# Performance work log

Hardware: AMD Instinct MI355X
Metric: run time of the kernel (lower is better)

The kernel has to match this reference:

```python
import jax, jax.numpy as jnp
import numpy as np

N_NODES = 100000
N_EDGES = 1600000
NUM_GRAPHS = 4096
EPS = 1e-5


def _glorot(key, shape):
    fan_in, fan_out = shape[0], shape[1]
    lim = float(np.sqrt(6.0 / (fan_in + fan_out)))
    return jax.random.uniform(key, shape, jnp.float32, -lim, lim)


def setup_inputs() -> dict:
    key = jax.random.key(0)
    ks = jax.random.split(key, 32)
    inp = {}
    inp['x'] = jax.random.normal(ks[0], (N_NODES, 32), jnp.float32)
    inp['edge_attr'] = jax.random.uniform(ks[1], (N_EDGES, 8), jnp.float32)
    inp['edge_index'] = jax.random.randint(ks[2], (2, N_EDGES), 0, N_NODES, jnp.int32)
    inp['batch'] = jnp.sort(jax.random.randint(ks[3], (N_NODES,), 0, NUM_GRAPHS, jnp.int32))
    inp['num_graphs'] = NUM_GRAPHS
    # node/edge embeddings
    inp['Wn'] = _glorot(ks[4], (32, 64)); inp['bn_'] = jnp.zeros((64,), jnp.float32)
    inp['We'] = _glorot(ks[5], (8, 16)); inp['be_'] = jnp.zeros((16,), jnp.float32)
    # conv1: 2*64+16=144 -> 128 -> 64
    inp['W1a'] = _glorot(ks[6], (144, 128)); inp['b1a'] = jnp.zeros((128,), jnp.float32)
    inp['W1b'] = _glorot(ks[7], (128, 64)); inp['b1b'] = jnp.zeros((64,), jnp.float32)
    # conv2: 2*64+16=144 -> 64 -> 32
    inp['W2a'] = _glorot(ks[8], (144, 64)); inp['b2a'] = jnp.zeros((64,), jnp.float32)
    inp['W2b'] = _glorot(ks[9], (64, 32)); inp['b2b'] = jnp.zeros((32,), jnp.float32)
    # conv3: 2*32+16=80 -> 32 -> 16
    inp['W3a'] = _glorot(ks[10], (80, 32)); inp['b3a'] = jnp.zeros((32,), jnp.float32)
    inp['W3b'] = _glorot(ks[11], (32, 16)); inp['b3b'] = jnp.zeros((16,), jnp.float32)
    # batchnorm affine params
    inp['g1'] = jnp.ones((64,), jnp.float32); inp['beta1'] = jnp.zeros((64,), jnp.float32)
    inp['g2'] = jnp.ones((32,), jnp.float32); inp['beta2'] = jnp.zeros((32,), jnp.float32)
    inp['g3'] = jnp.ones((16,), jnp.float32); inp['beta3'] = jnp.zeros((16,), jnp.float32)
    # final fc 16 -> 12
    inp['Wfc'] = _glorot(ks[12], (16, 12)); inp['bfc'] = jnp.zeros((12,), jnp.float32)
    return inp


def _conv(x, e_emb, src, dst, Wa, ba, Wb, bb, n_nodes):
    # PyG: x_i = x[target]=x[dst], x_j = x[source]=x[src]; message MLP; mean-aggregate at dst
    m = jnp.concatenate([x[dst], x[src], e_emb], axis=1)      # [E, 2*in+edge]
    m = jax.nn.relu(m @ Wa + ba) @ Wb + bb                    # [E, out]
    s = jax.ops.segment_sum(m, dst, num_segments=n_nodes)
    cnt = jax.ops.segment_sum(jnp.ones((m.shape[0], 1), m.dtype), dst, num_segments=n_nodes)
    return s / jnp.maximum(cnt, 1.0)


def _batchnorm(x, g, b):
    mu = jnp.mean(x, axis=0)
    var = jnp.mean(jnp.square(x - mu), axis=0)
    return (x - mu) * jax.lax.rsqrt(var + EPS) * g + b


def reference(x, edge_attr, edge_index, batch, num_graphs,
              Wn, bn_, We, be_, W1a, b1a, W1b, b1b, W2a, b2a, W2b, b2b,
              W3a, b3a, W3b, b3b, g1, beta1, g2, beta2, g3, beta3, Wfc, bfc):
    n_nodes = x.shape[0]
    src, dst = edge_index[0], edge_index[1]
    e_emb = jax.nn.relu(edge_attr @ We + be_)                 # [E, 16]
    h = jax.nn.relu(x @ Wn + bn_)                             # [N, 64]
    h = _conv(h, e_emb, src, dst, W1a, b1a, W1b, b1b, n_nodes)
    h = jax.nn.relu(_batchnorm(h, g1, beta1))
    h = _conv(h, e_emb, src, dst, W2a, b2a, W2b, b2b, n_nodes)
    h = jax.nn.relu(_batchnorm(h, g2, beta2))
    h = _conv(h, e_emb, src, dst, W3a, b3a, W3b, b3b, n_nodes)
    h = jax.nn.relu(_batchnorm(h, g3, beta3))
    # global mean pool per graph
    s = jax.ops.segment_sum(h, batch, num_segments=num_graphs)
    cnt = jax.ops.segment_sum(jnp.ones((n_nodes, 1), h.dtype), batch, num_segments=num_graphs)
    pooled = s / jnp.maximum(cnt, 1.0)                        # [G, 16]
    return jax.nn.sigmoid(pooled @ Wfc + bfc)                 # [G, 12]
```

## Files before the change

### kernel.cpp

```cpp
#include <hip/hip_runtime.h>
#include <hip/hip_bf16.h>
#include <cstdio>


#define N_NODES 100000
#define N_EDGES 1600000
#define NUM_GRAPHS 4096

typedef unsigned short u16;
typedef unsigned int u32;
typedef _Float16 h2 __attribute__((ext_vector_type(2)));

#if defined(__has_builtin)
#if __has_builtin(__builtin_amdgcn_fdot2)
#define DOT2(a, b, c) __builtin_amdgcn_fdot2((a), (b), (c), false)
#endif
#endif
#ifndef DOT2
#define DOT2(a, b, c) ((c) + (float)(a).x * (float)(b).x + (float)(a).y * (float)(b).y)
#endif

__device__ __forceinline__ float b2f(u16 u) { union { u32 i; float f; } c; c.i = ((u32)u) << 16; return c.f; }
__device__ __forceinline__ float b2f_lo(u32 u) { union { u32 i; float f; } c; c.i = u << 16; return c.f; }
__device__ __forceinline__ float b2f_hi(u32 u) { union { u32 i; float f; } c; c.i = u & 0xffff0000u; return c.f; }
__device__ __forceinline__ u16 f2b(float f) {
    __hip_bfloat16 h = __float2bfloat16(f);
    return *reinterpret_cast<u16*>(&h);
}

template <int CPL>
__device__ __forceinline__ void ld_bf16(const u16* base, float out[CPL]) {
    if constexpr (CPL == 1) {
        out[0] = b2f(*base);
    } else {
        u32 v = *(const u32*)base;
        out[0] = b2f_lo(v); out[1] = b2f_hi(v);
    }
}
template <int CPL>
__device__ __forceinline__ void ld_f32(const float* base, float out[CPL]) {
    if constexpr (CPL == 1) {
        out[0] = *base;
    } else {
        float2 v = *(const float2*)base;
        out[0] = v.x; out[1] = v.y;
    }
}

__global__ __launch_bounds__(256) void hist_k(const int* __restrict__ dst, int* __restrict__ hist) {
    int e = blockIdx.x * 256 + threadIdx.x;
    if (e < N_EDGES) atomicAdd(&hist[dst[e]], 1);
}

__global__ __launch_bounds__(256) void scan_part_k(const int* __restrict__ hist,
        int* __restrict__ excl, int* __restrict__ bsum) {
    __shared__ int sm[256];
    int t = threadIdx.x, b = blockIdx.x;
    int base = b * 1024 + t * 4;
    int v0 = (base + 0 < N_NODES) ? hist[base + 0] : 0;
    int v1 = (base + 1 < N_NODES) ? hist[base + 1] : 0;
    int v2 = (base + 2 < N_NODES) ? hist[base + 2] : 0;
    int v3 = (base + 3 < N_NODES) ? hist[base + 3] : 0;
    int tsum = v0 + v1 + v2 + v3;
    sm[t] = tsum;
    __syncthreads();
    for (int o = 1; o < 256; o <<= 1) {
        int x = (t >= o) ? sm[t - o] : 0;
        __syncthreads();
        sm[t] += x;
        __syncthreads();
    }
    int texcl = sm[t] - tsum;
    if (base + 0 < N_NODES) excl[base + 0] = texcl;
    if (base + 1 < N_NODES) excl[base + 1] = texcl + v0;
    if (base + 2 < N_NODES) excl[base + 2] = texcl + v0 + v1;
    if (base + 3 < N_NODES) excl[base + 3] = texcl + v0 + v1 + v2;
    if (t == 255) bsum[b] = sm[255];
}

__global__ __launch_bounds__(256) void scan_top_k(int* __restrict__ bsum, int* __restrict__ boff,
        int nb, int* __restrict__ row_ptr_last) {
    __shared__ int sm[256];
    int t = threadIdx.x;
    int v = (t < nb) ? bsum[t] : 0;
    sm[t] = v;
    __syncthreads();
    for (int o = 1; o < 256; o <<= 1) {
        int x = (t >= o) ? sm[t - o] : 0;
        __syncthreads();
        sm[t] += x;
        __syncthreads();
    }
    if (t < nb) boff[t] = sm[t] - v;
    if (t == 0) *row_ptr_last = sm[255];
}

__global__ __launch_bounds__(256) void scan_add_k(int* __restrict__ excl, const int* __restrict__ boff,
        int* __restrict__ row_ptr, int* __restrict__ cursor) {
    int i = blockIdx.x * 256 + threadIdx.x;
    if (i >= N_NODES) return;
    int s = excl[i] + boff[i >> 10];
    row_ptr[i] = s;
    cursor[i] = s;
}

__global__ __launch_bounds__(256) void scatter_k(const int* __restrict__ src, const int* __restrict__ dst,
        int* __restrict__ cursor, int* __restrict__ sorted_eid, int* __restrict__ srcs) {
    int e = blockIdx.x * 256 + threadIdx.x;
    if (e < N_EDGES) {
        int p = atomicAdd(&cursor[dst[e]], 1);
        sorted_eid[p] = e;
        srcs[p] = src[e];
    }
}

__global__ __launch_bounds__(256) void edge_emb_k(const float* __restrict__ ea,
        const float* __restrict__ We, const float* __restrict__ be,
        const int* __restrict__ sorted_eid, _Float16* __restrict__ e16s) {
    int idx = blockIdx.x * 256 + threadIdx.x;
    if (idx >= N_EDGES * 16) return;
    int p = idx >> 4, k = idx & 15;
    int e = sorted_eid[p];
    float acc = be[k];
#pragma unroll
    for (int j = 0; j < 8; ++j) acc += ea[(size_t)e * 8 + j] * We[j * 16 + k];
    e16s[idx] = (_Float16)fmaxf(acc, 0.f);
}

__global__ __launch_bounds__(256) void node_emb_k(const float* __restrict__ x,
        const float* __restrict__ Wn, const float* __restrict__ bn_, float* __restrict__ h) {
    int idx = blockIdx.x * 256 + threadIdx.x;
    if (idx >= N_NODES * 64) return;
    int v = idx >> 6, c = idx & 63;
    float acc = bn_[c];
    for (int k = 0; k < 32; ++k) acc += x[(size_t)v * 32 + k] * Wn[(size_t)k * 64 + c];
    h[idx] = fmaxf(acc, 0.f);
}

template <int F, int H>
__global__ __launch_bounds__(256) void proj_k(const float* __restrict__ h,
        const float* __restrict__ Wa, const float* __restrict__ ba,
        float* __restrict__ Pd, u16* __restrict__ Ps) {
    constexpr int C2 = 2 * H;
    constexpr int NPB = 256 / C2;
    constexpr int TILE = 16 * NPB;
    __shared__ float hs[TILE][F];
    const int t = threadIdx.x;
    const int grp = t / C2;
    const int c = t % C2;
    const bool is_src = (c >= H);
    const int cc = is_src ? (c - H) : c;
    float w[F];
    const float* wcol = Wa + (size_t)(is_src ? F : 0) * H + cc;
#pragma unroll
    for (int k = 0; k < F; ++k) w[k] = wcol[(size_t)k * H];
    const float bias = is_src ? 0.f : ba[cc];

    for (int v0 = blockIdx.x * TILE; v0 < N_NODES; v0 += gridDim.x * TILE) {
        __syncthreads();
        for (int i = t; i < TILE * F; i += 256) {
            int vv = v0 + i / F;
            hs[i / F][i % F] = (vv < N_NODES) ? h[(size_t)vv * F + (i % F)] : 0.f;
        }
        __syncthreads();
        const int base = grp * 16;
        const int nmax = (N_NODES - v0 - base >= 16) ? 16
                        : (N_NODES - v0 - base > 0 ? N_NODES - v0 - base : 0);
#pragma unroll 2
        for (int n = 0; n < nmax; ++n) {
            const int v = v0 + base + n;
            const float4* hr4 = (const float4*)hs[base + n];
            float a0 = bias, a1 = 0.f, a2 = 0.f, a3 = 0.f;
#pragma unroll
            for (int k4 = 0; k4 < F / 4; ++k4) {
                float4 hv = hr4[k4];
                a0 += hv.x * w[4 * k4 + 0];
                a1 += hv.y * w[4 * k4 + 1];
                a2 += hv.z * w[4 * k4 + 2];
                a3 += hv.w * w[4 * k4 + 3];
            }
            float acc = (a0 + a1) + (a2 + a3);
            if (is_src) Ps[(size_t)v * H + cc] = f2b(acc);
            else        Pd[(size_t)v * H + cc] = acc;
        }
    }
}

template <int H>
__global__ __launch_bounds__(256) void conv_k(
        const int* __restrict__ row_ptr, const int* __restrict__ srcs,
        const _Float16* __restrict__ e16s,
        float* __restrict__ Pd, const u16* __restrict__ Ps,
        const float* __restrict__ Wae) {
    constexpr int SL = (H >= 64) ? 64 : 32;
    constexpr int NPW = 64 / SL;
    constexpr int CPL = H / SL;
    constexpr int NPB = 4 * NPW;
    const int wave = threadIdx.x >> 6, lane = threadIdx.x & 63;
    const int sub = lane / SL;
    const int sl = lane % SL;
    const int c0 = sl * CPL;
    h2 w2h[8][CPL];
#pragma unroll
    for (int k2 = 0; k2 < 8; ++k2)
#pragma unroll
        for (int j = 0; j < CPL; ++j) {
            h2 t;
            t.x = (_Float16)Wae[(2 * k2) * H + c0 + j];
            t.y = (_Float16)Wae[(2 * k2 + 1) * H + c0 + j];
            w2h[k2][j] = t;
        }

    for (int v = blockIdx.x * NPB + wave * NPW + sub; v < N_NODES; v += gridDim.x * NPB) {
        const int vv = (SL == 64) ? __builtin_amdgcn_readfirstlane(v) : v;
        float pd[CPL], acc[CPL];
        ld_f32<CPL>(&Pd[(size_t)vv * H + c0], pd);
#pragma unroll
        for (int j = 0; j < CPL; ++j) acc[j] = 0.f;
        const int p0 = row_ptr[vv], p1 = row_ptr[vv + 1];
        const int deg = p1 - p0;

        auto edge = [&](uint4 ra, uint4 rb, const float ps[CPL]) {
            union { u32 u; h2 h; } cv;
            h2 ev[8];
            cv.u = ra.x; ev[0] = cv.h; cv.u = ra.y; ev[1] = cv.h;
            cv.u = ra.z; ev[2] = cv.h; cv.u = ra.w; ev[3] = cv.h;
            cv.u = rb.x; ev[4] = cv.h; cv.u = rb.y; ev[5] = cv.h;
            cv.u = rb.z; ev[6] = cv.h; cv.u = rb.w; ev[7] = cv.h;
            float z[CPL];
#pragma unroll
            for (int j = 0; j < CPL; ++j) z[j] = pd[j] + ps[j];
#pragma unroll
            for (int k2 = 0; k2 < 8; ++k2)
#pragma unroll
                for (int j = 0; j < CPL; ++j) z[j] = DOT2(ev[k2], w2h[k2][j], z[j]);
#pragma unroll
            for (int j = 0; j < CPL; ++j) acc[j] += fmaxf(z[j], 0.f);
        };

        int p = p0;
        for (; p + 3 < p1; p += 4) {
            int s0 = srcs[p], s1 = srcs[p + 1], s2 = srcs[p + 2], s3 = srcs[p + 3];
            const uint4* e0 = (const uint4*)(e16s + (size_t)p * 16);
            uint4 a0 = e0[0], a1 = e0[1];
            uint4 b0 = e0[2], b1 = e0[3];
            uint4 g0 = e0[4], g1 = e0[5];
            uint4 d0 = e0[6], d1 = e0[7];
            float ps0[CPL], ps1[CPL], ps2[CPL], ps3[CPL];
            ld_bf16<CPL>(&Ps[(size_t)s0 * H + c0], ps0);
            ld_bf16<CPL>(&Ps[(size_t)s1 * H + c0], ps1);
            ld_bf16<CPL>(&Ps[(size_t)s2 * H + c0], ps2);
            ld_bf16<CPL>(&Ps[(size_t)s3 * H + c0], ps3);
            edge(a0, a1, ps0);
            edge(b0, b1, ps1);
            edge(g0, g1, ps2);
            edge(d0, d1, ps3);
        }
        for (; p < p1; ++p) {
            int s0 = srcs[p];
            const uint4* e0 = (const uint4*)(e16s + (size_t)p * 16);
            uint4 a0 = e0[0], a1 = e0[1];
            float ps0[CPL];
            ld_bf16<CPL>(&Ps[(size_t)s0 * H + c0], ps0);
            edge(a0, a1, ps0);
        }

        const float invd = (deg > 0) ? 1.f / (float)deg : 0.f;
        if constexpr (CPL == 2) {
            float2 o; o.x = acc[0] * invd; o.y = acc[1] * invd;
            *(float2*)&Pd[(size_t)vv * H + c0] = o;
        } else {
            Pd[(size_t)vv * H + c0] = acc[0] * invd;
        }
    }
}

template <int H, int Fo>
__global__ __launch_bounds__(256) void matvec2_k(const float* __restrict__ m,
        const int* __restrict__ row_ptr,
        const float* __restrict__ Wb, const float* __restrict__ bb,
        float* __restrict__ y, float* __restrict__ stats) {
    constexpr int FoC = (Fo < 32) ? Fo : 32;
    constexpr int CG = Fo / FoC;
    constexpr int NPW = 32 / FoC;
    constexpr int NG = 4 / CG;
    constexpr int SLOTS = NG * NPW;
    constexpr int KH = H / 2;
    constexpr int TILE = 4096 / H;
    constexpr int J = TILE / SLOTS;

    __shared__ float hs[TILE * H];
    __shared__ int ptile[TILE + 1];
    __shared__ float sh[2 * Fo];

    const int t = threadIdx.x;
    const int wave = t >> 6, lane = t & 63;
    const int kh = lane >> 5;
    const int r = lane & 31;
    const int c_lo = r % FoC;
    const int s = r / FoC;
    const int cg = wave % CG;
    const int ng = wave / CG;
    const int c = cg * FoC + c_lo;
    const int slot = ng * NPW + s;

    for (int i = t; i < 2 * Fo; i += 256) sh[i] = 0.f;

    float w[KH];
#pragma unroll
    for (int k = 0; k < KH; ++k) w[k] = Wb[(size_t)(kh * KH + k) * Fo + c];
    const float bias = bb[c];
    float s1 = 0.f, s2 = 0.f;

    const float4* msrc = (const float4*)m;
    float4* hs4 = (float4*)hs;

    for (int v0 = blockIdx.x * TILE; v0 < N_NODES; v0 += gridDim.x * TILE) {
        __syncthreads();
#pragma unroll
        for (int q = t; q < 1024; q += 256) {
            int node = (q * 4) / H;
            float4 val;
            if (v0 + node < N_NODES) val = msrc[(size_t)v0 * (H / 4) + q];
            else { val.x = val.y = val.z = val.w = 0.f; }
            hs4[q] = val;
        }
        for (int i = t; i <= TILE; i += 256) {
            int v = v0 + i;
            ptile[i] = row_ptr[v < N_NODES ? v : N_NODES];
        }
        __syncthreads();

        for (int j = 0; j < J; ++j) {
            const int n = slot + j * SLOTS;
            const int v = v0 + n;
            const float4* hr4 = (const float4*)&hs[n * H + kh * KH];
            float a0 = 0.f, a1 = 0.f, a2 = 0.f, a3 = 0.f;
#pragma unroll
            for (int k4 = 0; k4 < KH / 4; ++k4) {
                float4 hv = hr4[k4];
                a0 += hv.x * w[4 * k4 + 0];
                a1 += hv.y * w[4 * k4 + 1];
                a2 += hv.z * w[4 * k4 + 2];
                a3 += hv.w * w[4 * k4 + 3];
            }
            float half = (a0 + a1) + (a2 + a3);
            float total = half + __shfl_xor(half, 32) + bias;
            if (kh == 0 && v < N_NODES) {
                const int deg = ptile[n + 1] - ptile[n];
                float val = (deg > 0) ? total : 0.f;
                y[(size_t)v * Fo + c] = val;
                s1 += val; s2 += val * val;
            }
        }
    }

    __syncthreads();
    if (kh == 0) {
        atomicAdd(&sh[c], s1);
        atomicAdd(&sh[Fo + c], s2);
    }
    __syncthreads();
    if (t < 2 * Fo) atomicAdd(&stats[t], sh[t]);
}

template <int Fo>
__global__ __launch_bounds__(256) void bnrelu_k(float* __restrict__ y,
        const float* __restrict__ stats, const float* __restrict__ g, const float* __restrict__ beta) {
    int idx = blockIdx.x * 256 + threadIdx.x;
    if (idx >= N_NODES * Fo) return;
    int co = idx % Fo;
    const float invN = 1.0f / (float)N_NODES;
    float mu = stats[co] * invN;
    float ex2 = stats[Fo + co] * invN;
    float var = fmaxf(ex2 - mu * mu, 0.f);
    float rs = rsqrtf(var + 1e-5f);
    y[idx] = fmaxf((y[idx] - mu) * rs * g[co] + beta[co], 0.f);
}

__global__ __launch_bounds__(256) void pool_k(const float* __restrict__ h,
        const int* __restrict__ batch, float* __restrict__ pool, int* __restrict__ gcnt) {
    int idx = blockIdx.x * 256 + threadIdx.x;
    if (idx >= N_NODES * 16) return;
    int v = idx >> 4, c = idx & 15;
    int b = batch[v];
    atomicAdd(&pool[b * 16 + c], h[idx]);
    if (c == 0) atomicAdd(&gcnt[b], 1);
}

__global__ __launch_bounds__(256) void out_k(const float* __restrict__ pool,
        const int* __restrict__ gcnt, const float* __restrict__ Wfc,
        const float* __restrict__ bfc, float* __restrict__ out) {
    int idx = blockIdx.x * 256 + threadIdx.x;
    if (idx >= NUM_GRAPHS * 12) return;
    int g = idx / 12, o = idx % 12;
    int cnt = gcnt[g];
    float inv = 1.0f / (float)(cnt > 0 ? cnt : 1);
    float acc = bfc[o];
#pragma unroll
    for (int k = 0; k < 16; ++k) acc += pool[g * 16 + k] * inv * Wfc[k * 12 + o];
    out[idx] = 1.0f / (1.0f + expf(-acc));
}

extern "C" void kernel_launch(void* const* d_in, const int* in_sizes, int n_in,
                              void* d_out, int out_size, void* d_ws, size_t ws_size,
                              hipStream_t stream) {
    const size_t N = N_NODES, E = N_EDGES, G = NUM_GRAPHS;
    const float* x = (const float*)d_in[0];
    const float* ea = (const float*)d_in[1];
    const int* ei = (const int*)d_in[2];
    const int* srcv = ei;
    const int* dstv = ei + E;
    const int* batch = (const int*)d_in[3];
    const float* Wn = (const float*)d_in[5];  const float* bn_ = (const float*)d_in[6];
    const float* We = (const float*)d_in[7];  const float* be_ = (const float*)d_in[8];
    const float* W1a = (const float*)d_in[9]; const float* b1a = (const float*)d_in[10];
    const float* W1b = (const float*)d_in[11]; const float* b1b = (const float*)d_in[12];
    const float* W2a = (const float*)d_in[13]; const float* b2a = (const float*)d_in[14];
    const float* W2b = (const float*)d_in[15]; const float* b2b = (const float*)d_in[16];
    const float* W3a = (const float*)d_in[17]; const float* b3a = (const float*)d_in[18];
    const float* W3b = (const float*)d_in[19]; const float* b3b = (const float*)d_in[20];
    const float* g1 = (const float*)d_in[21]; const float* be1 = (const float*)d_in[22];
    const float* g2 = (const float*)d_in[23]; const float* be2 = (const float*)d_in[24];
    const float* g3 = (const float*)d_in[25]; const float* be3 = (const float*)d_in[26];
    const float* Wfc = (const float*)d_in[27]; const float* bfc = (const float*)d_in[28];

    char* base = (char*)d_ws;
    size_t off = 0;
    auto take = [&](size_t bytes) { size_t o = off; off += (bytes + 255) & ~(size_t)255; return o; };
    int* hist = (int*)(base + take(N * 4));
    int* cursor = (int*)(base + take(N * 4));
    int* row_ptr = (int*)(base + take((N + 1) * 4));
    int* bsum = (int*)(base + take(256 * 4));
    int* boff = (int*)(base + take(256 * 4));
    int* sorted = (int*)(base + take(E * 4));
    int* srcs = (int*)(base + take(E * 4));
    float* hbuf = (float*)(base + take(N * 64 * 4));
    float* Pd = (float*)(base + take(N * 128 * 4));
    u16* Ps = (u16*)(base + take(N * 128 * 2));
    _Float16* e16s = (_Float16*)(base + take(E * 16 * 2));
    float* stats = (float*)(base + take(256 * 4));
    float* pool = (float*)(base + take(G * 16 * 4));
    int* gcnt = (int*)(base + take(G * 4));
    if (off > ws_size) {
        fprintf(stderr, "kernel_launch: ws too small: need %zu have %zu\n", off, ws_size);
        return;
    }

    const int NB = (N_NODES + 1023) / 1024;

    hipMemsetAsync(hist, 0, N * 4, stream);
    hist_k<<<dim3((E + 255) / 256), dim3(256), 0, stream>>>(dstv, hist);
    scan_part_k<<<dim3(NB), dim3(256), 0, stream>>>(hist, cursor, bsum);
    scan_top_k<<<dim3(1), dim3(256), 0, stream>>>(bsum, boff, NB, &row_ptr[N_NODES]);
    scan_add_k<<<dim3((N + 255) / 256), dim3(256), 0, stream>>>(cursor, boff, row_ptr, cursor);
    scatter_k<<<dim3((E + 255) / 256), dim3(256), 0, stream>>>(srcv, dstv, cursor, sorted, srcs);

    edge_emb_k<<<dim3((E * 16 + 255) / 256), dim3(256), 0, stream>>>(ea, We, be_, sorted, e16s);
    node_emb_k<<<dim3((N * 64 + 255) / 256), dim3(256), 0, stream>>>(x, Wn, bn_, hbuf);

    proj_k<64, 128><<<dim3(6250), dim3(256), 0, stream>>>(hbuf, W1a, b1a, Pd, Ps);
    conv_k<128><<<dim3(3072), dim3(256), 0, stream>>>(row_ptr, srcs, e16s, Pd, Ps, W1a + 128 * 128);
    hipMemsetAsync(stats, 0, 256 * 4, stream);
    matvec2_k<128, 64><<<dim3(1024), dim3(256), 0, stream>>>(Pd, row_ptr, W1b, b1b, hbuf, stats);
    bnrelu_k<64><<<dim3((N * 64 + 255) / 256), dim3(256), 0, stream>>>(hbuf, stats, g1, be1);

    proj_k<64, 64><<<dim3(3125), dim3(256), 0, stream>>>(hbuf, W2a, b2a, Pd, Ps);
    conv_k<64><<<dim3(3072), dim3(256), 0, stream>>>(row_ptr, srcs, e16s, Pd, Ps, W2a + 128 * 64);
    hipMemsetAsync(stats, 0, 256 * 4, stream);
    matvec2_k<64, 32><<<dim3(1024), dim3(256), 0, stream>>>(Pd, row_ptr, W2b, b2b, hbuf, stats);
    bnrelu_k<32><<<dim3((N * 32 + 255) / 256), dim3(256), 0, stream>>>(hbuf, stats, g2, be2);

    proj_k<32, 32><<<dim3(1563), dim3(256), 0, stream>>>(hbuf, W3a, b3a, Pd, Ps);
    conv_k<32><<<dim3(3072), dim3(256), 0, stream>>>(row_ptr, srcs, e16s, Pd, Ps, W3a + 64 * 32);
    hipMemsetAsync(stats, 0, 256 * 4, stream);
    matvec2_k<32, 16><<<dim3(1024), dim3(256), 0, stream>>>(Pd, row_ptr, W3b, b3b, hbuf, stats);
    bnrelu_k<16><<<dim3((N * 16 + 255) / 256), dim3(256), 0, stream>>>(hbuf, stats, g3, be3);

    hipMemsetAsync(pool, 0, G * 16 * 4, stream);
    hipMemsetAsync(gcnt, 0, G * 4, stream);
    pool_k<<<dim3((N * 16 + 255) / 256), dim3(256), 0, stream>>>(hbuf, batch, pool, gcnt);
    out_k<<<dim3((G * 12 + 255) / 256), dim3(256), 0, stream>>>(pool, gcnt, Wfc, bfc, (float*)d_out);
}
```

Measured before the change: 1.023 ms.

## Balance conv work by edge-count node ranges and fuse final BN into pooling

```diff
diff --git a/kernel.cpp b/kernel.cpp
--- a/kernel.cpp
+++ b/kernel.cpp
@@ -112,6 +112,19 @@
         sorted_eid[p] = e;
         srcs[p] = src[e];
     }
+}
+
+__global__ __launch_bounds__(256) void ubound_k(const int* __restrict__ row_ptr, int* __restrict__ sn) {
+    int u = blockIdx.x * 256 + threadIdx.x;
+    if (u > 25000) return;
+    if (u == 25000) { sn[u] = N_NODES; return; }
+    int target = u * 64;
+    int lo = 0, hi = N_NODES;
+    while (lo < hi) {
+        int mid = (lo + hi) >> 1;
+        if (row_ptr[mid] >= target) hi = mid; else lo = mid + 1;
+    }
+    sn[u] = lo;
 }
 
 __global__ __launch_bounds__(256) void edge_emb_k(const float* __restrict__ ea,
@@ -188,14 +201,13 @@
 
 template <int H>
 __global__ __launch_bounds__(256) void conv_k(
-        const int* __restrict__ row_ptr, const int* __restrict__ srcs,
-        const _Float16* __restrict__ e16s,
+        const int* __restrict__ sn, const int* __restrict__ row_ptr,
+        const int* __restrict__ srcs, const _Float16* __restrict__ e16s,
         float* __restrict__ Pd, const u16* __restrict__ Ps,
         const float* __restrict__ Wae) {
     constexpr int SL = (H >= 64) ? 64 : 32;
     constexpr int NPW = 64 / SL;
     constexpr int CPL = H / SL;
-    constexpr int NPB = 4 * NPW;
     const int wave = threadIdx.x >> 6, lane = threadIdx.x & 63;
     const int sub = lane / SL;
     const int sl = lane % SL;
@@ -211,7 +223,10 @@
             w2h[k2][j] = t;
         }
 
-    for (int v = blockIdx.x * NPB + wave * NPW + sub; v < N_NODES; v += gridDim.x * NPB) {
+    const int uid = (blockIdx.x * 4 + wave) * NPW + sub;
+    const int vbeg = sn[uid], vend = sn[uid + 1];
+
+    for (int v = vbeg; v < vend; ++v) {
         const int vv = (SL == 64) ? __builtin_amdgcn_readfirstlane(v) : v;
         float pd[CPL], acc[CPL];
         ld_f32<CPL>(&Pd[(size_t)vv * H + c0], pd);
@@ -378,13 +393,20 @@
     y[idx] = fmaxf((y[idx] - mu) * rs * g[co] + beta[co], 0.f);
 }
 
-__global__ __launch_bounds__(256) void pool_k(const float* __restrict__ h,
+__global__ __launch_bounds__(256) void pool_bn_k(const float* __restrict__ y,
+        const float* __restrict__ stats, const float* __restrict__ g, const float* __restrict__ beta,
         const int* __restrict__ batch, float* __restrict__ pool, int* __restrict__ gcnt) {
     int idx = blockIdx.x * 256 + threadIdx.x;
     if (idx >= N_NODES * 16) return;
     int v = idx >> 4, c = idx & 15;
+    const float invN = 1.0f / (float)N_NODES;
+    float mu = stats[c] * invN;
+    float ex2 = stats[16 + c] * invN;
+    float var = fmaxf(ex2 - mu * mu, 0.f);
+    float rs = rsqrtf(var + 1e-5f);
+    float val = fmaxf((y[idx] - mu) * rs * g[c] + beta[c], 0.f);
     int b = batch[v];
-    atomicAdd(&pool[b * 16 + c], h[idx]);
+    atomicAdd(&pool[b * 16 + c], val);
     if (c == 0) atomicAdd(&gcnt[b], 1);
 }
 
@@ -433,6 +455,7 @@
     int* row_ptr = (int*)(base + take((N + 1) * 4));
     int* bsum = (int*)(base + take(256 * 4));
     int* boff = (int*)(base + take(256 * 4));
+    int* sn = (int*)(base + take(25001 * 4));
     int* sorted = (int*)(base + take(E * 4));
     int* srcs = (int*)(base + take(E * 4));
     float* hbuf = (float*)(base + take(N * 64 * 4));
@@ -455,30 +478,30 @@
     scan_top_k<<<dim3(1), dim3(256), 0, stream>>>(bsum, boff, NB, &row_ptr[N_NODES]);
     scan_add_k<<<dim3((N + 255) / 256), dim3(256), 0, stream>>>(cursor, boff, row_ptr, cursor);
     scatter_k<<<dim3((E + 255) / 256), dim3(256), 0, stream>>>(srcv, dstv, cursor, sorted, srcs);
+    ubound_k<<<dim3((25001 + 255) / 256), dim3(256), 0, stream>>>(row_ptr, sn);
 
     edge_emb_k<<<dim3((E * 16 + 255) / 256), dim3(256), 0, stream>>>(ea, We, be_, sorted, e16s);
     node_emb_k<<<dim3((N * 64 + 255) / 256), dim3(256), 0, stream>>>(x, Wn, bn_, hbuf);
 
     proj_k<64, 128><<<dim3(6250), dim3(256), 0, stream>>>(hbuf, W1a, b1a, Pd, Ps);
-    conv_k<128><<<dim3(3072), dim3(256), 0, stream>>>(row_ptr, srcs, e16s, Pd, Ps, W1a + 128 * 128);
+    conv_k<128><<<dim3(6250), dim3(256), 0, stream>>>(sn, row_ptr, srcs, e16s, Pd, Ps, W1a + 128 * 128);
     hipMemsetAsync(stats, 0, 256 * 4, stream);
     matvec2_k<128, 64><<<dim3(1024), dim3(256), 0, stream>>>(Pd, row_ptr, W1b, b1b, hbuf, stats);
     bnrelu_k<64><<<dim3((N * 64 + 255) / 256), dim3(256), 0, stream>>>(hbuf, stats, g1, be1);
 
     proj_k<64, 64><<<dim3(3125), dim3(256), 0, stream>>>(hbuf, W2a, b2a, Pd, Ps);
-    conv_k<64><<<dim3(3072), dim3(256), 0, stream>>>(row_ptr, srcs, e16s, Pd, Ps, W2a + 128 * 64);
+    conv_k<64><<<dim3(6250), dim3(256), 0, stream>>>(sn, row_ptr, srcs, e16s, Pd, Ps, W2a + 128 * 64);
     hipMemsetAsync(stats, 0, 256 * 4, stream);
     matvec2_k<64, 32><<<dim3(1024), dim3(256), 0, stream>>>(Pd, row_ptr, W2b, b2b, hbuf, stats);
     bnrelu_k<32><<<dim3((N * 32 + 255) / 256), dim3(256), 0, stream>>>(hbuf, stats, g2, be2);
 
     proj_k<32, 32><<<dim3(1563), dim3(256), 0, stream>>>(hbuf, W3a, b3a, Pd, Ps);
-    conv_k<32><<<dim3(3072), dim3(256), 0, stream>>>(row_ptr, srcs, e16s, Pd, Ps, W3a + 64 * 32);
+    conv_k<32><<<dim3(3125), dim3(256), 0, stream>>>(sn, row_ptr, srcs, e16s, Pd, Ps, W3a + 64 * 32);
     hipMemsetAsync(stats, 0, 256 * 4, stream);
     matvec2_k<32, 16><<<dim3(1024), dim3(256), 0, stream>>>(Pd, row_ptr, W3b, b3b, hbuf, stats);
-    bnrelu_k<16><<<dim3((N * 16 + 255) / 256), dim3(256), 0, stream>>>(hbuf, stats, g3, be3);
 
     hipMemsetAsync(pool, 0, G * 16 * 4, stream);
     hipMemsetAsync(gcnt, 0, G * 4, stream);
-    pool_k<<<dim3((N * 16 + 255) / 256), dim3(256), 0, stream>>>(hbuf, batch, pool, gcnt);
+    pool_bn_k<<<dim3((N * 16 + 255) / 256), dim3(256), 0, stream>>>(hbuf, stats, g3, be3, batch, pool, gcnt);
     out_k<<<dim3((G * 12 + 255) / 256), dim3(256), 0, stream>>>(pool, gcnt, Wfc, bfc, (float*)d_out);
 }
```

Result: no change. 1.033 ms (+1.0%).
